# Kernel tuning notes

Measured on AMD Instinct MI355X. Metric: run time of the kernel, lower is better.

Reference implementation:

```python
import jax, jax.numpy as jnp
import numpy as np

N = 100000
H = 256
E = 3200000
L = 4


def setup_inputs() -> dict:
    key = jax.random.key(0)
    ks = jax.random.split(key, 5)
    x = jax.random.normal(ks[0], (N, H), dtype=jnp.float32)
    edge_index = jax.random.randint(ks[1], (2, E), 0, N, dtype=jnp.int64)
    scale = 1.0 / np.sqrt(H)
    # PyG SAGEConv per layer: lin_l (applied to aggregated neighbors, with bias)
    # and lin_r (root/self weight, no bias). Stack the 4 layers.
    Wl = jax.random.normal(ks[2], (L, H, H), dtype=jnp.float32) * scale
    Wr = jax.random.normal(ks[3], (L, H, H), dtype=jnp.float32) * scale
    b = jax.random.normal(ks[4], (L, H), dtype=jnp.float32) * 0.01
    return {"x": x, "edge_index": edge_index, "Wl": Wl, "Wr": Wr, "b": b}


def _sage_conv(x, src, dst, Wl, Wr, b):
    # mean aggregation of source-node features onto destination nodes
    msg = x[src]                                   # [E, H] gather
    agg = jax.ops.segment_sum(msg, dst, num_segments=N)   # [N, H] scatter-add
    cnt = jax.ops.segment_sum(jnp.ones((src.shape[0],), x.dtype), dst,
                              num_segments=N)      # [N] in-degree
    mean = agg / jnp.maximum(cnt, 1.0)[:, None]
    # out = lin_l(mean) + lin_r(x);  torch Linear: y = x @ W.T + b
    return mean @ Wl.T + b + x @ Wr.T


def reference(x, edge_index, Wl, Wr, b):
    src, dst = edge_index[0], edge_index[1]
    h = x
    for l in range(L):
        h = _sage_conv(h, src, dst, Wl[l], Wr[l], b[l])
        if l < L - 1:
            h = jax.nn.relu(h)
    return h
```

## Files before the change

### kernel.cpp

```cpp
#include <hip/hip_runtime.h>

#define kN 100000
#define kH 256
#define kE 3200000
#define kL 4

typedef __attribute__((ext_vector_type(8))) short bf16x8;
typedef __attribute__((ext_vector_type(4))) float f32x4;

static __device__ __forceinline__ float b2f(unsigned short u) {
    return __uint_as_float(((unsigned int)u) << 16);
}
static __device__ __forceinline__ unsigned short f2b(float f) {
    unsigned int u = __float_as_uint(f);
    u = (u + 0x7fffu + ((u >> 16) & 1u)) >> 16;
    return (unsigned short)u;
}

static __device__ __forceinline__ int is_i64(const int* flags) { return flags[0] == 0; }
static __device__ __forceinline__ int is_bf(const int* flags) { return flags[1] > (1 << 15); }

static __device__ __forceinline__ int eidx(const int* __restrict__ ei, int i64, int pos) {
    return i64 ? ei[2 * pos] : ei[pos];
}

__global__ __launch_bounds__(256) void detect_kernel(const unsigned int* __restrict__ eiw,
                                                     const unsigned short* __restrict__ xu,
                                                     int* __restrict__ flags) {
    __shared__ int scount[4];
    int t = blockIdx.x * 256 + threadIdx.x;
    int lane = threadIdx.x & 63, wave = threadIdx.x >> 6;
    unsigned int eor = 0;
#pragma unroll
    for (int j = 0; j < 16; ++j) eor |= eiw[(size_t)t * 32 + 2 * j + 1];
    for (int off = 32; off >= 1; off >>= 1) eor |= __shfl_down(eor, off);
    if (lane == 0 && eor) atomicOr(&flags[0], 1);
    unsigned short u = xu[2 * t];
    unsigned int e = (u >> 7) & 0xFF;
    unsigned long long m = __ballot(e >= 101 && e <= 140);
    if (lane == 0) scount[wave] = (int)__popcll(m);
    __syncthreads();
    if (threadIdx.x == 0)
        atomicAdd(&flags[1], scount[0] + scount[1] + scount[2] + scount[3]);
}

__global__ __launch_bounds__(256) void conv_x_kernel(const void* __restrict__ x,
                                                     unsigned short* __restrict__ xb,
                                                     const int* __restrict__ flags) {
    int i = (blockIdx.x * 256 + threadIdx.x) * 4;
    if (is_bf(flags)) {
        *(ushort4*)&xb[i] = *(const ushort4*)&((const unsigned short*)x)[i];
    } else {
        float4 v = *(const float4*)&((const float*)x)[i];
        ushort4 o;
        o.x = f2b(v.x); o.y = f2b(v.y); o.z = f2b(v.z); o.w = f2b(v.w);
        *(ushort4*)&xb[i] = o;
    }
}

__global__ __launch_bounds__(256) void conv_w_kernel(const void* __restrict__ Wl,
                                                     const void* __restrict__ Wr,
                                                     unsigned short* __restrict__ wlb,
                                                     unsigned short* __restrict__ wrb,
                                                     const int* __restrict__ flags) {
    int i = (blockIdx.x * 256 + threadIdx.x) * 4;
    if (is_bf(flags)) {
        *(ushort4*)&wlb[i] = *(const ushort4*)&((const unsigned short*)Wl)[i];
        *(ushort4*)&wrb[i] = *(const ushort4*)&((const unsigned short*)Wr)[i];
    } else {
        float4 a = *(const float4*)&((const float*)Wl)[i];
        float4 b = *(const float4*)&((const float*)Wr)[i];
        ushort4 oa, ob;
        oa.x = f2b(a.x); oa.y = f2b(a.y); oa.z = f2b(a.z); oa.w = f2b(a.w);
        ob.x = f2b(b.x); ob.y = f2b(b.y); ob.z = f2b(b.z); ob.w = f2b(b.w);
        *(ushort4*)&wlb[i] = oa;
        *(ushort4*)&wrb[i] = ob;
    }
}

__global__ __launch_bounds__(256) void conv_b_kernel(const void* __restrict__ b,
                                                     float* __restrict__ biasf,
                                                     const int* __restrict__ flags) {
    int i = threadIdx.x * 4;
    if (is_bf(flags)) {
        ushort4 u = *(const ushort4*)&((const unsigned short*)b)[i];
        biasf[i + 0] = b2f(u.x); biasf[i + 1] = b2f(u.y);
        biasf[i + 2] = b2f(u.z); biasf[i + 3] = b2f(u.w);
    } else {
        *(float4*)&biasf[i] = *(const float4*)&((const float*)b)[i];
    }
}

__global__ __launch_bounds__(256) void hist_kernel(const int* __restrict__ ei,
                                                   const int* __restrict__ flags,
                                                   int* __restrict__ deg) {
    int e = blockIdx.x * 256 + threadIdx.x;
    if (e < kE) atomicAdd(&deg[eidx(ei, is_i64(flags), kE + e)], 1);
}

__global__ __launch_bounds__(256) void scan1_kernel(const int* __restrict__ deg,
                                                    int* __restrict__ rowstart,
                                                    int* __restrict__ blocksum) {
    __shared__ int sdata[256];
    int t = threadIdx.x;
    int base = blockIdx.x * 1024 + t * 4;
    int v[4]; int s = 0;
#pragma unroll
    for (int i = 0; i < 4; ++i) {
        v[i] = (base + i < kN) ? deg[base + i] : 0;
        s += v[i];
    }
    sdata[t] = s;
    __syncthreads();
    for (int off = 1; off < 256; off <<= 1) {
        int x = (t >= off) ? sdata[t - off] : 0;
        __syncthreads();
        sdata[t] += x;
        __syncthreads();
    }
    int run = sdata[t] - s;
    if (t == 255) blocksum[blockIdx.x] = sdata[255];
#pragma unroll
    for (int i = 0; i < 4; ++i) {
        if (base + i < kN) rowstart[base + i] = run;
        run += v[i];
    }
}

__global__ void scan2_kernel(int* __restrict__ blocksum, int nb) {
    if (threadIdx.x == 0 && blockIdx.x == 0) {
        int acc = 0;
        for (int i = 0; i < nb; ++i) { int t = blocksum[i]; blocksum[i] = acc; acc += t; }
    }
}

__global__ __launch_bounds__(256) void scan3_kernel(int* __restrict__ rowstart,
                                                    const int* __restrict__ blocksum,
                                                    const int* __restrict__ deg,
                                                    int* __restrict__ cursor,
                                                    float* __restrict__ inv_cnt) {
    int i = blockIdx.x * 256 + threadIdx.x;
    if (i < kN) {
        int rs = rowstart[i] + blocksum[i >> 10];
        rowstart[i] = rs;
        cursor[i] = rs;
        int d = deg[i];
        inv_cnt[i] = 1.0f / (float)(d > 0 ? d : 1);
    }
}

__global__ __launch_bounds__(256) void fill_kernel(const int* __restrict__ ei,
                                                   const int* __restrict__ flags,
                                                   int* __restrict__ cursor,
                                                   int* __restrict__ colidx) {
    int e = blockIdx.x * 256 + threadIdx.x;
    if (e < kE) {
        int i64 = is_i64(flags);
        int s = eidx(ei, i64, e);
        int d = eidx(ei, i64, kE + e);
        int p = atomicAdd(&cursor[d], 1);
        colidx[p] = s;
    }
}

__global__ __launch_bounds__(256) void agg_kernel(const unsigned short* __restrict__ h,
                                                  const int* __restrict__ rowstart,
                                                  const int* __restrict__ deg,
                                                  const float* __restrict__ inv_cnt,
                                                  const int* __restrict__ colidx,
                                                  unsigned short* __restrict__ mean) {
    int node = blockIdx.x * 4 + (threadIdx.x >> 6);
    int lane = threadIdx.x & 63;
    int start = rowstart[node];
    int d = deg[node];
    float a0 = 0.f, a1 = 0.f, a2 = 0.f, a3 = 0.f;
    int j = 0;
    for (; j + 4 <= d; j += 4) {
        int c0 = colidx[start + j + 0];
        int c1 = colidx[start + j + 1];
        int c2 = colidx[start + j + 2];
        int c3 = colidx[start + j + 3];
        ushort4 v0 = *(const ushort4*)&h[c0 * kH + lane * 4];
        ushort4 v1 = *(const ushort4*)&h[c1 * kH + lane * 4];
        ushort4 v2 = *(const ushort4*)&h[c2 * kH + lane * 4];
        ushort4 v3 = *(const ushort4*)&h[c3 * kH + lane * 4];
        a0 += b2f(v0.x) + b2f(v1.x) + b2f(v2.x) + b2f(v3.x);
        a1 += b2f(v0.y) + b2f(v1.y) + b2f(v2.y) + b2f(v3.y);
        a2 += b2f(v0.z) + b2f(v1.z) + b2f(v2.z) + b2f(v3.z);
        a3 += b2f(v0.w) + b2f(v1.w) + b2f(v2.w) + b2f(v3.w);
    }
    for (; j < d; ++j) {
        int c = colidx[start + j];
        ushort4 v = *(const ushort4*)&h[c * kH + lane * 4];
        a0 += b2f(v.x); a1 += b2f(v.y); a2 += b2f(v.z); a3 += b2f(v.w);
    }
    float ic = inv_cnt[node];
    ushort4 o;
    o.x = f2b(a0 * ic); o.y = f2b(a1 * ic); o.z = f2b(a2 * ic); o.w = f2b(a3 * ic);
    *(ushort4*)&mean[node * kH + lane * 4] = o;
}

#define BM 128
#define BN 64
#define BK 64
#define LDA 72
#define LDB 72

__global__ __launch_bounds__(256) void gemm_kernel(const unsigned short* __restrict__ mean,
                                                   const unsigned short* __restrict__ h,
                                                   const unsigned short* __restrict__ Wlb,
                                                   const unsigned short* __restrict__ Wrb,
                                                   const float* __restrict__ biasf,
                                                   unsigned short* __restrict__ hout,
                                                   float* __restrict__ foutf,
                                                   unsigned short* __restrict__ foutu,
                                                   const int* __restrict__ flags,
                                                   int is_final) {
    __shared__ __align__(16) unsigned short sA[BM * LDA];
    __shared__ __align__(16) unsigned short sB[BN * LDB];
    int bm0 = blockIdx.x * BM;
    int bn0 = blockIdx.y * BN;
    int tid = threadIdx.x;
    int wave = tid >> 6, lane = tid & 63;
    int quad = lane >> 4, r16 = lane & 15;

    f32x4 acc[2][4] = {};

    for (int kb = 0; kb < 512; kb += BK) {
        const unsigned short* Asrc = (kb < 256) ? mean : h;
        const unsigned short* Wsrc = (kb < 256) ? Wlb : Wrb;
        int kcol = kb & 255;
#pragma unroll
        for (int i = 0; i < 8; ++i) {
            int v = tid + i * 256;
            int row = v >> 4, c4 = (v & 15) * 4;
            int grow = bm0 + row;
            ushort4 val;
            if (grow < kN) val = *(const ushort4*)&Asrc[grow * kH + kcol + c4];
            else { val.x = val.y = val.z = val.w = 0; }
            *(ushort4*)&sA[row * LDA + c4] = val;
        }
#pragma unroll
        for (int i = 0; i < 4; ++i) {
            int v = tid + i * 256;
            int row = v >> 4, c4 = (v & 15) * 4;
            int gn = bn0 + row;
            *(ushort4*)&sB[row * LDB + c4] = *(const ushort4*)&Wsrc[gn * kH + kcol + c4];
        }
        __syncthreads();

#pragma unroll
        for (int ko = 0; ko < 2; ++ko) {
            bf16x8 af[2], bfv[4];
#pragma unroll
            for (int mt = 0; mt < 2; ++mt)
                af[mt] = *(const bf16x8*)&sA[(wave * 32 + mt * 16 + r16) * LDA + ko * 32 + quad * 8];
#pragma unroll
            for (int nt = 0; nt < 4; ++nt)
                bfv[nt] = *(const bf16x8*)&sB[(nt * 16 + r16) * LDB + ko * 32 + quad * 8];
#pragma unroll
            for (int mt = 0; mt < 2; ++mt)
#pragma unroll
                for (int nt = 0; nt < 4; ++nt)
                    acc[mt][nt] = __builtin_amdgcn_mfma_f32_16x16x32_bf16(
                        af[mt], bfv[nt], acc[mt][nt], 0, 0, 0);
        }
        __syncthreads();
    }

    int bf = is_bf(flags);
#pragma unroll
    for (int mt = 0; mt < 2; ++mt) {
        int mbase = bm0 + wave * 32 + mt * 16 + quad * 4;
#pragma unroll
        for (int nt = 0; nt < 4; ++nt) {
            int n = bn0 + nt * 16 + r16;
            float bv = biasf[n];
#pragma unroll
            for (int i = 0; i < 4; ++i) {
                int m = mbase + i;
                if (m < kN) {
                    float v = acc[mt][nt][i] + bv;
                    if (!is_final) {
                        v = fmaxf(v, 0.f);
                        hout[m * kH + n] = f2b(v);
                    } else if (bf) {
                        foutu[m * kH + n] = f2b(v);
                    } else {
                        foutf[m * kH + n] = v;
                    }
                }
            }
        }
    }
}

extern "C" void kernel_launch(void* const* d_in, const int* in_sizes, int n_in,
                              void* d_out, int out_size, void* d_ws, size_t ws_size,
                              hipStream_t stream) {
    const void* x  = d_in[0];
    const int*  ei = (const int*)d_in[1];
    const void* Wl = d_in[2];
    const void* Wr = d_in[3];
    const void* bb = d_in[4];

    char* p = (char*)d_ws;
    int*   flags    = (int*)p;   p += 1024;
    int*   colidx   = (int*)p;   p += (size_t)kE * 4;
    int*   rowstart = (int*)p;   p += (size_t)kN * 4;
    int*   deg      = (int*)p;   p += (size_t)kN * 4;
    int*   cursor   = (int*)p;   p += (size_t)kN * 4;
    float* inv_cnt  = (float*)p; p += (size_t)kN * 4;
    int*   blocksum = (int*)p;   p += 4096;
    float* biasf    = (float*)p; p += (size_t)kL * kH * 4;
    unsigned short* wlb   = (unsigned short*)p; p += (size_t)kL * kH * kH * 2;
    unsigned short* wrb   = (unsigned short*)p; p += (size_t)kL * kH * kH * 2;
    unsigned short* xb    = (unsigned short*)p; p += (size_t)kN * kH * 2;
    unsigned short* h0    = (unsigned short*)p; p += (size_t)kN * kH * 2;
    unsigned short* meanb = (unsigned short*)p; p += (size_t)kN * kH * 2;

    hipMemsetAsync(flags, 0, 1024, stream);
    hipMemsetAsync(deg, 0, (size_t)kN * 4, stream);

    detect_kernel<<<256, 256, 0, stream>>>((const unsigned int*)ei,
                                           (const unsigned short*)x, flags);
    conv_x_kernel<<<(kN * kH / 4 + 255) / 256, 256, 0, stream>>>(x, xb, flags);
    conv_w_kernel<<<(kL * kH * kH / 4 + 255) / 256, 256, 0, stream>>>(Wl, Wr, wlb, wrb, flags);
    conv_b_kernel<<<1, 256, 0, stream>>>(bb, biasf, flags);

    hist_kernel<<<(kE + 255) / 256, 256, 0, stream>>>(ei, flags, deg);
    int nb = (kN + 1023) / 1024;
    scan1_kernel<<<nb, 256, 0, stream>>>(deg, rowstart, blocksum);
    scan2_kernel<<<1, 64, 0, stream>>>(blocksum, nb);
    scan3_kernel<<<(kN + 255) / 256, 256, 0, stream>>>(rowstart, blocksum, deg, cursor, inv_cnt);
    fill_kernel<<<(kE + 255) / 256, 256, 0, stream>>>(ei, flags, cursor, colidx);

    const unsigned short* hcur = xb;
    for (int l = 0; l < kL; ++l) {
        agg_kernel<<<kN / 4, 256, 0, stream>>>(hcur, rowstart, deg, inv_cnt, colidx, meanb);
        int is_final = (l == kL - 1);
        unsigned short* hout = (l & 1) ? xb : h0;
        gemm_kernel<<<dim3((kN + BM - 1) / BM, kH / BN), 256, 0, stream>>>(
            meanb, hcur,
            wlb + (size_t)l * kH * kH, wrb + (size_t)l * kH * kH,
            biasf + (size_t)l * kH,
            hout, (float*)d_out, (unsigned short*)d_out, flags, is_final);
        hcur = hout;
    }
}
```

Before: 1.955 ms.

## Build CSR with two-pass bucketed counting sort instead of global atomics

Replaces the global-atomic histogram and fill passes with a two-level counting sort. Edges are first binned by destination into buckets of 256 nodes using shared-memory atomics and a global scan over per-block counts, then each bucket is sorted locally in shared memory to produce rowstart, degree, inverse counts and column indices. This removes millions of contended global atomics and improves locality of the colidx writes, at the cost of extra passes over an intermediate pair buffer that is aliased onto the feature workspaces. Edge order within a row is no longer deterministic, so floating-point sums may change slightly.

```diff
diff --git a/kernel.cpp b/kernel.cpp
--- a/kernel.cpp
+++ b/kernel.cpp
@@ -4,6 +4,11 @@
 #define kH 256
 #define kE 3200000
 #define kL 4
+
+#define NB   391
+#define EPB  8192
+#define NBLK 391
+#define NC   (NB * NBLK)
 
 typedef __attribute__((ext_vector_type(8))) short bf16x8;
 typedef __attribute__((ext_vector_type(4))) float f32x4;
@@ -91,23 +96,32 @@
     }
 }
 
-__global__ __launch_bounds__(256) void hist_kernel(const int* __restrict__ ei,
+__global__ __launch_bounds__(256) void binA_kernel(const int* __restrict__ ei,
                                                    const int* __restrict__ flags,
-                                                   int* __restrict__ deg) {
-    int e = blockIdx.x * 256 + threadIdx.x;
-    if (e < kE) atomicAdd(&deg[eidx(ei, is_i64(flags), kE + e)], 1);
-}
-
-__global__ __launch_bounds__(256) void scan1_kernel(const int* __restrict__ deg,
-                                                    int* __restrict__ rowstart,
-                                                    int* __restrict__ blocksum) {
+                                                   int* __restrict__ counts) {
+    __shared__ int hist[NB];
+    for (int i = threadIdx.x; i < NB; i += 256) hist[i] = 0;
+    __syncthreads();
+    int i64 = is_i64(flags);
+    int base = blockIdx.x * EPB;
+    int end = min(kE, base + EPB);
+    for (int e = base + threadIdx.x; e < end; e += 256)
+        atomicAdd(&hist[eidx(ei, i64, kE + e) >> 8], 1);
+    __syncthreads();
+    for (int i = threadIdx.x; i < NB; i += 256)
+        counts[i * NBLK + blockIdx.x] = hist[i];
+}
+
+__global__ __launch_bounds__(256) void gscan1_kernel(const int* __restrict__ counts,
+                                                     int* __restrict__ offs,
+                                                     int* __restrict__ blocksum) {
     __shared__ int sdata[256];
     int t = threadIdx.x;
     int base = blockIdx.x * 1024 + t * 4;
     int v[4]; int s = 0;
 #pragma unroll
     for (int i = 0; i < 4; ++i) {
-        v[i] = (base + i < kN) ? deg[base + i] : 0;
+        v[i] = (base + i < NC) ? counts[base + i] : 0;
         s += v[i];
     }
     sdata[t] = s;
@@ -122,44 +136,85 @@
     if (t == 255) blocksum[blockIdx.x] = sdata[255];
 #pragma unroll
     for (int i = 0; i < 4; ++i) {
-        if (base + i < kN) rowstart[base + i] = run;
+        if (base + i < NC) offs[base + i] = run;
         run += v[i];
     }
 }
 
-__global__ void scan2_kernel(int* __restrict__ blocksum, int nb) {
+__global__ void gscan2_kernel(int* __restrict__ blocksum, int nb) {
     if (threadIdx.x == 0 && blockIdx.x == 0) {
         int acc = 0;
         for (int i = 0; i < nb; ++i) { int t = blocksum[i]; blocksum[i] = acc; acc += t; }
     }
 }
 
-__global__ __launch_bounds__(256) void scan3_kernel(int* __restrict__ rowstart,
-                                                    const int* __restrict__ blocksum,
-                                                    const int* __restrict__ deg,
-                                                    int* __restrict__ cursor,
-                                                    float* __restrict__ inv_cnt) {
+__global__ __launch_bounds__(256) void gscan3_kernel(int* __restrict__ offs,
+                                                     const int* __restrict__ blocksum) {
     int i = blockIdx.x * 256 + threadIdx.x;
-    if (i < kN) {
-        int rs = rowstart[i] + blocksum[i >> 10];
-        rowstart[i] = rs;
-        cursor[i] = rs;
-        int d = deg[i];
-        inv_cnt[i] = 1.0f / (float)(d > 0 ? d : 1);
-    }
-}
-
-__global__ __launch_bounds__(256) void fill_kernel(const int* __restrict__ ei,
+    if (i < NC) offs[i] += blocksum[i >> 10];
+}
+
+__global__ __launch_bounds__(256) void binC_kernel(const int* __restrict__ ei,
                                                    const int* __restrict__ flags,
-                                                   int* __restrict__ cursor,
-                                                   int* __restrict__ colidx) {
-    int e = blockIdx.x * 256 + threadIdx.x;
-    if (e < kE) {
-        int i64 = is_i64(flags);
+                                                   const int* __restrict__ offs,
+                                                   uint2* __restrict__ pairs) {
+    __shared__ int cur[NB];
+    for (int i = threadIdx.x; i < NB; i += 256)
+        cur[i] = offs[i * NBLK + blockIdx.x];
+    __syncthreads();
+    int i64 = is_i64(flags);
+    int base = blockIdx.x * EPB;
+    int end = min(kE, base + EPB);
+    for (int e = base + threadIdx.x; e < end; e += 256) {
         int s = eidx(ei, i64, e);
         int d = eidx(ei, i64, kE + e);
-        int p = atomicAdd(&cursor[d], 1);
-        colidx[p] = s;
+        int p = atomicAdd(&cur[d >> 8], 1);
+        uint2 pr; pr.x = (unsigned)s; pr.y = (unsigned)d;
+        pairs[p] = pr;
+    }
+}
+
+__global__ __launch_bounds__(256) void binD_kernel(const uint2* __restrict__ pairs,
+                                                   const int* __restrict__ offs,
+                                                   int* __restrict__ rowstart,
+                                                   int* __restrict__ deg,
+                                                   float* __restrict__ inv_cnt,
+                                                   int* __restrict__ colidx) {
+    __shared__ int cnt[256];
+    __shared__ int sdata[256];
+    __shared__ int cur[256];
+    int b = blockIdx.x;
+    int t = threadIdx.x;
+    int node0 = b << 8;
+    int Ob = offs[b * NBLK];
+    int Oe = (b + 1 < NB) ? offs[(b + 1) * NBLK] : kE;
+    cnt[t] = 0;
+    __syncthreads();
+    for (int i = Ob + t; i < Oe; i += 256)
+        atomicAdd(&cnt[pairs[i].y - node0], 1);
+    __syncthreads();
+    int v = cnt[t];
+    sdata[t] = v;
+    __syncthreads();
+    for (int off = 1; off < 256; off <<= 1) {
+        int x = (t >= off) ? sdata[t - off] : 0;
+        __syncthreads();
+        sdata[t] += x;
+        __syncthreads();
+    }
+    int pfx = sdata[t] - v;
+    int node = node0 + t;
+    if (node < kN) {
+        rowstart[node] = Ob + pfx;
+        deg[node] = v;
+        inv_cnt[node] = 1.0f / (float)(v > 0 ? v : 1);
+    }
+    cur[t] = Ob + pfx;
+    __syncthreads();
+    for (int i = Ob + t; i < Oe; i += 256) {
+        uint2 pr = pairs[i];
+        int p = atomicAdd(&cur[pr.y - node0], 1);
+        colidx[p] = (int)pr.x;
     }
 }
 
@@ -309,7 +364,6 @@
     int*   colidx   = (int*)p;   p += (size_t)kE * 4;
     int*   rowstart = (int*)p;   p += (size_t)kN * 4;
     int*   deg      = (int*)p;   p += (size_t)kN * 4;
-    int*   cursor   = (int*)p;   p += (size_t)kN * 4;
     float* inv_cnt  = (float*)p; p += (size_t)kN * 4;
     int*   blocksum = (int*)p;   p += 4096;
     float* biasf    = (float*)p; p += (size_t)kL * kH * 4;
@@ -319,8 +373,11 @@
     unsigned short* h0    = (unsigned short*)p; p += (size_t)kN * kH * 2;
     unsigned short* meanb = (unsigned short*)p; p += (size_t)kN * kH * 2;
 
+    uint2* pairs  = (uint2*)meanb;
+    int*   counts = (int*)h0;
+    int*   offs   = (int*)h0 + NC;
+
     hipMemsetAsync(flags, 0, 1024, stream);
-    hipMemsetAsync(deg, 0, (size_t)kN * 4, stream);
 
     detect_kernel<<<256, 256, 0, stream>>>((const unsigned int*)ei,
                                            (const unsigned short*)x, flags);
@@ -328,12 +385,13 @@
     conv_w_kernel<<<(kL * kH * kH / 4 + 255) / 256, 256, 0, stream>>>(Wl, Wr, wlb, wrb, flags);
     conv_b_kernel<<<1, 256, 0, stream>>>(bb, biasf, flags);
 
-    hist_kernel<<<(kE + 255) / 256, 256, 0, stream>>>(ei, flags, deg);
-    int nb = (kN + 1023) / 1024;
-    scan1_kernel<<<nb, 256, 0, stream>>>(deg, rowstart, blocksum);
-    scan2_kernel<<<1, 64, 0, stream>>>(blocksum, nb);
-    scan3_kernel<<<(kN + 255) / 256, 256, 0, stream>>>(rowstart, blocksum, deg, cursor, inv_cnt);
-    fill_kernel<<<(kE + 255) / 256, 256, 0, stream>>>(ei, flags, cursor, colidx);
+    binA_kernel<<<NBLK, 256, 0, stream>>>(ei, flags, counts);
+    int nb2 = (NC + 1023) / 1024;
+    gscan1_kernel<<<nb2, 256, 0, stream>>>(counts, offs, blocksum);
+    gscan2_kernel<<<1, 64, 0, stream>>>(blocksum, nb2);
+    gscan3_kernel<<<(NC + 255) / 256, 256, 0, stream>>>(offs, blocksum);
+    binC_kernel<<<NBLK, 256, 0, stream>>>(ei, flags, offs, pairs);
+    binD_kernel<<<NB, 256, 0, stream>>>(pairs, offs, rowstart, deg, inv_cnt, colidx);
 
     const unsigned short* hcur = xb;
     for (int l = 0; l < kL; ++l) {
```

After: 1.652 ms. 1.18x faster.
